# Kernel tuning notes

Measured on AMD Instinct MI355X. Metric: run time of the kernel, lower is better.

Reference implementation:

```python
import jax, jax.numpy as jnp
import numpy as np

V, D, C, H = 32, 128, 2048, 8
B, M = 8, 2048
HD = D // H


def rms_norm(x, scale):
    # Whole-tensor (per-batch) RMS over dims (1,2), as in the source (quirky but faithful).
    Bx, Mx, Dx = x.shape
    fr = jnp.sqrt(jnp.sum(x * x, axis=(1, 2))) * (Mx * Dx) ** -0.5  # (B,)
    raw = x / fr[:, None, None]
    return scale[:Mx, :][None, :, :] * raw


def rope_tables(Mx):
    i = jnp.arange(D // 2, dtype=jnp.float32)
    # NOTE: faithful to source: exponent uses (i-1), not i.
    base = jnp.power(10000.0, -2.0 * (i - 1.0) / D)  # (D/2,)
    pos = jnp.arange(Mx, dtype=jnp.float32)
    ang = pos[:, None] * base[None, :]  # (M, D/2)
    return jnp.cos(ang), jnp.sin(ang)


def apply_rope(t, cos, sin):
    # Equivalent to bmm with the block-diagonal 2x2 rotation matrices:
    # out[2i]   =  t[2i]*cos + t[2i+1]*sin
    # out[2i+1] = -t[2i]*sin + t[2i+1]*cos
    te, to = t[..., 0::2], t[..., 1::2]
    oe = te * cos + to * sin
    oo = -te * sin + to * cos
    return jnp.stack([oe, oo], axis=-1).reshape(t.shape)


def mha(q, k, v, in_w, in_b, out_w, out_b):
    Bx, Mx, _ = q.shape
    qp = q @ in_w[:D].T + in_b[:D]
    kp = k @ in_w[D:2 * D].T + in_b[D:2 * D]
    vp = v @ in_w[2 * D:].T + in_b[2 * D:]
    qh = qp.reshape(Bx, Mx, H, HD).transpose(0, 2, 1, 3)
    kh = kp.reshape(Bx, Mx, H, HD).transpose(0, 2, 1, 3)
    vh = vp.reshape(Bx, Mx, H, HD).transpose(0, 2, 1, 3)
    scores = jnp.einsum('bhqd,bhkd->bhqk', qh, kh) / jnp.sqrt(jnp.float32(HD))
    causal = jnp.tril(jnp.ones((Mx, Mx), dtype=bool))
    scores = jnp.where(causal[None, None], scores, -jnp.inf)
    probs = jax.nn.softmax(scores, axis=-1)  # dropout=0.1 in train mode; eval here
    o = jnp.einsum('bhqk,bhkd->bhqd', probs, vh)
    o = o.transpose(0, 2, 1, 3).reshape(Bx, Mx, D)
    return o @ out_w.T + out_b


def setup_inputs():
    key = jax.random.key(0)
    ks = jax.random.split(key, 12)
    s = 0.02
    return {
        'idx': jax.random.randint(ks[0], (B, M), 0, V),
        'targets': jax.random.randint(ks[1], (B, M), 0, V),
        'emb': jax.random.normal(ks[2], (V, D), jnp.float32) * s,
        'rms_scale': jnp.ones((C, D), jnp.float32),
        'Wq': jax.random.normal(ks[3], (D, D), jnp.float32) * s,
        'Wk': jax.random.normal(ks[4], (D, D), jnp.float32) * s,
        'Wv': jax.random.normal(ks[5], (D, D), jnp.float32) * s,
        'in_proj_w': jax.random.normal(ks[6], (3 * D, D), jnp.float32) * s,
        'in_proj_b': jnp.zeros((3 * D,), jnp.float32),
        'out_proj_w': jax.random.normal(ks[7], (D, D), jnp.float32) * s,
        'out_proj_b': jnp.zeros((D,), jnp.float32),
        'lin_w': jax.random.normal(ks[8], (D, D), jnp.float32) * s,
        'lin_b': jnp.zeros((D,), jnp.float32),
        'out_w': jax.random.normal(ks[9], (V, D), jnp.float32) * s,
        'out_b': jnp.zeros((V,), jnp.float32),
    }


def reference(idx, targets, emb, rms_scale, Wq, Wk, Wv, in_proj_w, in_proj_b,
              out_proj_w, out_proj_b, lin_w, lin_b, out_w, out_b):
    x = emb[idx]                                  # (B, M, D)
    x = rms_norm(x, rms_scale)
    Q = x @ Wq.T
    K = x @ Wk.T
    Vv = x @ Wv.T
    cos, sin = rope_tables(x.shape[1])
    q_out = apply_rope(Q, cos, sin)
    k_out = apply_rope(K, cos, sin)
    v_out = apply_rope(Vv, cos, sin)              # source rotates V too (faithful)
    x = x + mha(q_out, k_out, v_out, in_proj_w, in_proj_b, out_proj_w, out_proj_b)
    x = rms_norm(x, rms_scale)
    x = x + jax.nn.relu(x @ lin_w.T + lin_b)
    logits = x @ out_w.T + out_b                  # (B, M, V)
    logp = jax.nn.log_softmax(logits, axis=-1)
    nll = -jnp.take_along_axis(logp, targets[..., None], axis=-1)[..., 0]
    loss = jnp.mean(nll)
    return logits, loss
```

## Files before the change

kernel.cpp:

```cpp
#include <hip/hip_runtime.h>
#include <hip/hip_bf16.h>
#include <math.h>

#define Vv   32
#define Dd   128
#define Hh   8
#define Bb   8
#define Mm   2048
#define BM   (Bb*Mm)
#define NEL  (BM*Dd)
#define XNS  140
#define QKS  396

typedef _Float16 half4_t __attribute__((ext_vector_type(4)));
typedef _Float16 half8_t __attribute__((ext_vector_type(8)));
typedef __fp16   fp16x2  __attribute__((ext_vector_type(2)));
typedef float    float4_t __attribute__((ext_vector_type(4)));
#define MFMA16 __builtin_amdgcn_mfma_f32_16x16x16f16
#define MFMA32 __builtin_amdgcn_mfma_f32_16x16x32_f16

#if __has_builtin(__builtin_amdgcn_exp2f)
__device__ __forceinline__ float fexp2(float x) { return __builtin_amdgcn_exp2f(x); }
#else
__device__ __forceinline__ float fexp2(float x) { return __expf(x * 0.6931471805599453f); }
#endif

__global__ __launch_bounds__(256) void front_kernel(const float* __restrict__ Wq,
                                                    const float* __restrict__ Wk,
                                                    const float* __restrict__ Wv,
                                                    const float* __restrict__ in_w,
                                                    const float* __restrict__ out_pw,
                                                    const float* __restrict__ lin_w,
                                                    const float* __restrict__ out_w,
                                                    _Float16* __restrict__ Wh,
                                                    float* __restrict__ cosT,
                                                    float* __restrict__ sinT,
                                                    const int* __restrict__ idx,
                                                    const float* __restrict__ emb,
                                                    _Float16* __restrict__ Xh,
                                                    float* __restrict__ partials) {
    __shared__ float wsum[4];
    if (blockIdx.x < 1040) {
        int gid = blockIdx.x * 256 + threadIdx.x;
        if (gid < 135168) {
            const float* src;
            int i;
            if (gid < 131072) {
                int seg = gid >> 14; i = gid & 16383;
                src = seg == 0 ? Wq : seg == 1 ? Wk : seg == 2 ? Wv :
                      seg < 6 ? in_w + (size_t)(seg - 3) * 16384 :
                      seg == 6 ? out_pw : lin_w;
            } else { src = out_w; i = gid - 131072; }
            int tile = i >> 8, within = i & 255;
            int nt = tile >> 3, kk = tile & 7;
            int r = within >> 4, cc = within & 15;
            Wh[gid] = (_Float16)src[(nt * 16 + r) * 128 + kk * 16 + cc];
        } else {
            int rid = gid - 135168;
            int i = rid & 63, m = rid >> 6;
            float ex = -2.0f * ((float)i - 1.0f) / 128.0f;
            float basef = expf(ex * 9.210340371976184f);
            float ang = (float)m * basef;
            cosT[rid] = cosf(ang);
            sinT[rid] = sinf(ang);
        }
    } else {
        int blk = blockIdx.x - 1040;
        int gid = blk * 256 + threadIdx.x;
        int token = gid >> 5, t4 = gid & 31;
        float4 x = *(const float4*)(emb + (size_t)idx[token] * 128 + t4 * 4);
        half4_t o;
        o[0] = (_Float16)x.x; o[1] = (_Float16)x.y; o[2] = (_Float16)x.z; o[3] = (_Float16)x.w;
        *(half4_t*)(Xh + (size_t)gid * 4) = o;
        float v = x.x * x.x + x.y * x.y + x.z * x.z + x.w * x.w;
        #pragma unroll
        for (int off = 32; off; off >>= 1) v += __shfl_xor(v, off);
        int lane = threadIdx.x & 63, wave = threadIdx.x >> 6;
        if (lane == 0) wsum[wave] = v;
        __syncthreads();
        if (threadIdx.x == 0) partials[blk] = wsum[0] + wsum[1] + wsum[2] + wsum[3];
    }
}

__global__ __launch_bounds__(256) void gemm_qkvproj_kernel(const _Float16* __restrict__ xh,
                                                           const float* __restrict__ scale,
                                                           const float* __restrict__ part1,
                                                           const _Float16* __restrict__ Whqkv,
                                                           const _Float16* __restrict__ Whin,
                                                           const float* __restrict__ in_b,
                                                           const float* __restrict__ cosT,
                                                           const float* __restrict__ sinT,
                                                           _Float16* __restrict__ xnh,
                                                           _Float16* __restrict__ Qp,
                                                           _Float16* __restrict__ Kp,
                                                           _Float16* __restrict__ Vp) {
    __shared__ _Float16 xn[32 * XNS];
    __shared__ _Float16 qkv[32 * QKS];
    __shared__ float wsum0[4];
    int tid = threadIdx.x;
    int row0 = blockIdx.x * 32;
    {
        float v = part1[(row0 >> 11) * 256 + tid];
        #pragma unroll
        for (int off = 32; off; off >>= 1) v += __shfl_xor(v, off);
        if ((tid & 63) == 0) wsum0[tid >> 6] = v;
    }
    __syncthreads();
    float iv = 512.0f / sqrtf(wsum0[0] + wsum0[1] + wsum0[2] + wsum0[3]);
    {
        #pragma unroll
        for (int it = 0; it < 2; it++) {
            int idx = tid + it * 256;
            int rw = idx >> 4, c8 = (idx & 15) * 8;
            int m = (row0 + rw) & (Mm - 1);
            half8_t x8 = *(const half8_t*)(xh + (size_t)(row0 + rw) * 128 + c8);
            const float* sp = scale + (size_t)m * 128 + c8;
            float4 s0 = *(const float4*)sp;
            float4 s1 = *(const float4*)(sp + 4);
            half8_t o8;
            o8[0] = (_Float16)((float)x8[0] * iv * s0.x);
            o8[1] = (_Float16)((float)x8[1] * iv * s0.y);
            o8[2] = (_Float16)((float)x8[2] * iv * s0.z);
            o8[3] = (_Float16)((float)x8[3] * iv * s0.w);
            o8[4] = (_Float16)((float)x8[4] * iv * s1.x);
            o8[5] = (_Float16)((float)x8[5] * iv * s1.y);
            o8[6] = (_Float16)((float)x8[6] * iv * s1.z);
            o8[7] = (_Float16)((float)x8[7] * iv * s1.w);
            *(half8_t*)(xn + rw * XNS + c8) = o8;
            *(half8_t*)(xnh + (size_t)(row0 + rw) * 128 + c8) = o8;
        }
    }
    __syncthreads();
    int wave = tid >> 6, lane = tid & 63;
    int r = lane & 15, c = lane >> 4;
    int nb = wave * 96;
    int nb16 = wave * 6;
    int aoff = c * 8;
    int boff = r * 16 + (c & 1) * 8;
    int bsel = c >> 1;
    {
        half8_t af[2][4];
        #pragma unroll
        for (int rt = 0; rt < 2; rt++)
            #pragma unroll
            for (int kk = 0; kk < 4; kk++)
                af[rt][kk] = *(const half8_t*)(xn + (rt * 16 + r) * XNS + kk * 32 + aoff);
        float4_t acc[2][6];
        #pragma unroll
        for (int rt = 0; rt < 2; rt++)
            #pragma unroll
            for (int t = 0; t < 6; t++) acc[rt][t] = (float4_t){0.f, 0.f, 0.f, 0.f};
        #pragma unroll
        for (int kk = 0; kk < 4; kk++) {
            half8_t wf[6];
            #pragma unroll
            for (int t = 0; t < 6; t++)
                wf[t] = *(const half8_t*)(Whqkv + ((nb16 + t) * 8 + kk * 2 + bsel) * 256 + boff);
            #pragma unroll
            for (int t = 0; t < 6; t++) {
                acc[0][t] = MFMA32(af[0][kk], wf[t], acc[0][t], 0, 0, 0);
                acc[1][t] = MFMA32(af[1][kk], wf[t], acc[1][t], 0, 0, 0);
            }
        }
        #pragma unroll
        for (int rt = 0; rt < 2; rt++) {
            #pragma unroll
            for (int t = 0; t < 6; t++) {
                int n = nb + t * 16 + r;
                int ci = (n & 127) >> 1;
                #pragma unroll
                for (int reg = 0; reg < 4; reg++) {
                    int m2 = (row0 + rt * 16 + 4 * c + reg) & (Mm - 1);
                    float v = acc[rt][t][reg];
                    float vp = __shfl_xor(v, 1);
                    float cs = cosT[m2 * 64 + ci], sn = sinT[m2 * 64 + ci];
                    v = (n & 1) ? (-vp * sn + v * cs) : (v * cs + vp * sn);
                    qkv[(rt * 16 + 4 * c + reg) * QKS + n] = (_Float16)v;
                }
            }
        }
    }
    __syncthreads();
    {
        int seg_lo = nb >> 7;
        int seg_hi = (nb + 80) >> 7;
        half8_t aql[2][4], aqh[2][4];
        #pragma unroll
        for (int rt = 0; rt < 2; rt++)
            #pragma unroll
            for (int kk = 0; kk < 4; kk++) {
                aql[rt][kk] = *(const half8_t*)(qkv + (rt * 16 + r) * QKS + seg_lo * 128 + kk * 32 + aoff);
                aqh[rt][kk] = *(const half8_t*)(qkv + (rt * 16 + r) * QKS + seg_hi * 128 + kk * 32 + aoff);
            }
        float4_t acc[2][6];
        #pragma unroll
        for (int rt = 0; rt < 2; rt++)
            #pragma unroll
            for (int t = 0; t < 6; t++) acc[rt][t] = (float4_t){0.f, 0.f, 0.f, 0.f};
        #pragma unroll
        for (int kk = 0; kk < 4; kk++) {
            half8_t wf[6];
            #pragma unroll
            for (int t = 0; t < 6; t++) {
                int colg = nb + t * 16;
                int seg = colg >> 7;
                int ntl = (colg & 127) >> 4;
                wf[t] = *(const half8_t*)(Whin + ((seg * 8 + ntl) * 8 + kk * 2 + bsel) * 256 + boff);
            }
            #pragma unroll
            for (int t = 0; t < 6; t++) {
                int seg = (nb + t * 16) >> 7;
                acc[0][t] = MFMA32(seg == seg_lo ? aql[0][kk] : aqh[0][kk], wf[t], acc[0][t], 0, 0, 0);
                acc[1][t] = MFMA32(seg == seg_lo ? aql[1][kk] : aqh[1][kk], wf[t], acc[1][t], 0, 0, 0);
            }
        }
        int bb = row0 >> 11;
        #pragma unroll
        for (int rt = 0; rt < 2; rt++) {
            int t16 = ((row0 + rt * 16) & 2047) >> 4;
            #pragma unroll
            for (int t = 0; t < 6; t++) {
                int colg = nb + t * 16;
                int seg = colg >> 7;
                int h = (colg & 127) >> 4;
                size_t tb = ((size_t)(bb * 8 + h) * 128 + t16) * 256;
                float bv = in_b[colg + r];
                _Float16* dst = seg == 0 ? Qp : seg == 1 ? Kp : Vp;
                #pragma unroll
                for (int reg = 0; reg < 4; reg++) {
                    float v = acc[rt][t][reg] + bv;
                    int key = 4 * c + reg;
                    if (seg < 2) dst[tb + key * 16 + r] = (_Float16)v;
                    else         dst[tb + r * 16 + key] = (_Float16)v;
                }
            }
        }
    }
}

__global__ __launch_bounds__(256) void gemm_ep1_kernel(const _Float16* __restrict__ Oh,
                                                       const _Float16* __restrict__ W6,
                                                       const float* __restrict__ bias,
                                                       const _Float16* __restrict__ xnh,
                                                       _Float16* __restrict__ xresh,
                                                       float* __restrict__ partials) {
    __shared__ _Float16 At[32 * XNS];
    int tid = threadIdx.x;
    int row0 = blockIdx.x * 32;
    #pragma unroll
    for (int it = 0; it < 2; it++) {
        int idx = tid + it * 256;
        int rw = idx >> 4, c8 = (idx & 15) * 8;
        *(half8_t*)(At + rw * XNS + c8) = *(const half8_t*)(Oh + (size_t)(row0 + rw) * 128 + c8);
    }
    __syncthreads();
    int wave = tid >> 6, lane = tid & 63;
    int r = lane & 15, c = lane >> 4;
    int aoff = c * 8;
    int boff = r * 16 + (c & 1) * 8;
    int bsel = c >> 1;
    int n0 = wave * 32;
    half8_t af[2][4];
    #pragma unroll
    for (int rt = 0; rt < 2; rt++)
        #pragma unroll
        for (int kk = 0; kk < 4; kk++)
            af[rt][kk] = *(const half8_t*)(At + (rt * 16 + r) * XNS + kk * 32 + aoff);
    float4_t acc[2][2];
    #pragma unroll
    for (int rt = 0; rt < 2; rt++) {
        acc[rt][0] = (float4_t){0.f, 0.f, 0.f, 0.f};
        acc[rt][1] = (float4_t){0.f, 0.f, 0.f, 0.f};
    }
    #pragma unroll
    for (int kk = 0; kk < 4; kk++) {
        half8_t wf[2];
        wf[0] = *(const half8_t*)(W6 + ((wave * 2 + 0) * 8 + kk * 2 + bsel) * 256 + boff);
        wf[1] = *(const half8_t*)(W6 + ((wave * 2 + 1) * 8 + kk * 2 + bsel) * 256 + boff);
        #pragma unroll
        for (int t = 0; t < 2; t++) {
            acc[0][t] = MFMA32(af[0][kk], wf[t], acc[0][t], 0, 0, 0);
            acc[1][t] = MFMA32(af[1][kk], wf[t], acc[1][t], 0, 0, 0);
        }
    }
    float lssq = 0.f;
    #pragma unroll
    for (int rt = 0; rt < 2; rt++) {
        #pragma unroll
        for (int t = 0; t < 2; t++) {
            int n = n0 + t * 16 + r;
            float bv = bias[n];
            #pragma unroll
            for (int reg = 0; reg < 4; reg++) {
                int row = row0 + rt * 16 + 4 * c + reg;
                float v = acc[rt][t][reg] + bv + (float)xnh[(size_t)row * 128 + n];
                lssq += v * v;
                xresh[(size_t)row * 128 + n] = (_Float16)v;
            }
        }
    }
    #pragma unroll
    for (int off = 32; off; off >>= 1) lssq += __shfl_xor(lssq, off);
    __shared__ float wsum[4];
    if (lane == 0) wsum[wave] = lssq;
    __syncthreads();
    if (tid == 0) partials[blockIdx.x] = wsum[0] + wsum[1] + wsum[2] + wsum[3];
}

__global__ __launch_bounds__(256) void gemm_ep2_kernel(const _Float16* __restrict__ xresh,
                                                       const float* __restrict__ scale,
                                                       const float* __restrict__ part2,
                                                       const _Float16* __restrict__ W7,
                                                       const float* __restrict__ bias,
                                                       _Float16* __restrict__ ffoh) {
    __shared__ _Float16 At[32 * XNS];
    int tid = threadIdx.x;
    int row0 = blockIdx.x * 32;
    float pv = part2[(row0 >> 11) * 64 + (tid & 63)];
    #pragma unroll
    for (int off = 32; off; off >>= 1) pv += __shfl_xor(pv, off);
    float iv = 512.0f / sqrtf(pv);
    #pragma unroll
    for (int it = 0; it < 2; it++) {
        int idx = tid + it * 256;
        int rw = idx >> 4, c8 = (idx & 15) * 8;
        int m = (row0 + rw) & (Mm - 1);
        half8_t x8 = *(const half8_t*)(xresh + (size_t)(row0 + rw) * 128 + c8);
        const float* sp = scale + (size_t)m * 128 + c8;
        float4 s0 = *(const float4*)sp;
        float4 s1 = *(const float4*)(sp + 4);
        half8_t o8;
        o8[0] = (_Float16)((float)x8[0] * iv * s0.x);
        o8[1] = (_Float16)((float)x8[1] * iv * s0.y);
        o8[2] = (_Float16)((float)x8[2] * iv * s0.z);
        o8[3] = (_Float16)((float)x8[3] * iv * s0.w);
        o8[4] = (_Float16)((float)x8[4] * iv * s1.x);
        o8[5] = (_Float16)((float)x8[5] * iv * s1.y);
        o8[6] = (_Float16)((float)x8[6] * iv * s1.z);
        o8[7] = (_Float16)((float)x8[7] * iv * s1.w);
        *(half8_t*)(At + rw * XNS + c8) = o8;
    }
    __syncthreads();
    int wave = tid >> 6, lane = tid & 63;
    int r = lane & 15, c = lane >> 4;
    int aoff = c * 8;
    int boff = r * 16 + (c & 1) * 8;
    int bsel = c >> 1;
    int n0 = wave * 32;
    half8_t af[2][4];
    #pragma unroll
    for (int rt = 0; rt < 2; rt++)
        #pragma unroll
        for (int kk = 0; kk < 4; kk++)
            af[rt][kk] = *(const half8_t*)(At + (rt * 16 + r) * XNS + kk * 32 + aoff);
    float4_t acc[2][2];
    #pragma unroll
    for (int rt = 0; rt < 2; rt++) {
        acc[rt][0] = (float4_t){0.f, 0.f, 0.f, 0.f};
        acc[rt][1] = (float4_t){0.f, 0.f, 0.f, 0.f};
    }
    #pragma unroll
    for (int kk = 0; kk < 4; kk++) {
        half8_t wf[2];
        wf[0] = *(const half8_t*)(W7 + ((wave * 2 + 0) * 8 + kk * 2 + bsel) * 256 + boff);
        wf[1] = *(const half8_t*)(W7 + ((wave * 2 + 1) * 8 + kk * 2 + bsel) * 256 + boff);
        #pragma unroll
        for (int t = 0; t < 2; t++) {
            acc[0][t] = MFMA32(af[0][kk], wf[t], acc[0][t], 0, 0, 0);
            acc[1][t] = MFMA32(af[1][kk], wf[t], acc[1][t], 0, 0, 0);
        }
    }
    #pragma unroll
    for (int rt = 0; rt < 2; rt++) {
        #pragma unroll
        for (int t = 0; t < 2; t++) {
            int n = n0 + t * 16 + r;
            float bv = bias[n];
            #pragma unroll
            for (int reg = 0; reg < 4; reg++) {
                int row = row0 + rt * 16 + 4 * c + reg;
                float v = fmaxf(acc[rt][t][reg] + bv, 0.f) + (float)xresh[(size_t)row * 128 + n];
                ffoh[(size_t)row * 128 + n] = (_Float16)v;
            }
        }
    }
}

__device__ __forceinline__ half4_t attn_exps(float4_t st, float& ls) {
    float p0 = fexp2(st[0]), p1 = fexp2(st[1]);
    float p2 = fexp2(st[2]), p3 = fexp2(st[3]);
    ls += (p0 + p1) + (p2 + p3);
    fp16x2 lo = __builtin_amdgcn_cvt_pkrtz(p0, p1);
    fp16x2 hi = __builtin_amdgcn_cvt_pkrtz(p2, p3);
    half4_t pf;
    pf[0] = (_Float16)lo[0]; pf[1] = (_Float16)lo[1];
    pf[2] = (_Float16)hi[0]; pf[3] = (_Float16)hi[1];
    return pf;
}
__device__ __forceinline__ half4_t attn_exps_masked(float4_t st, float& ls, int r, int c) {
    float p0 = (4 * c + 0 <= r) ? fexp2(st[0]) : 0.f;
    float p1 = (4 * c + 1 <= r) ? fexp2(st[1]) : 0.f;
    float p2 = (4 * c + 2 <= r) ? fexp2(st[2]) : 0.f;
    float p3 = (4 * c + 3 <= r) ? fexp2(st[3]) : 0.f;
    ls += (p0 + p1) + (p2 + p3);
    fp16x2 lo = __builtin_amdgcn_cvt_pkrtz(p0, p1);
    fp16x2 hi = __builtin_amdgcn_cvt_pkrtz(p2, p3);
    half4_t pf;
    pf[0] = (_Float16)lo[0]; pf[1] = (_Float16)lo[1];
    pf[2] = (_Float16)hi[0]; pf[3] = (_Float16)hi[1];
    return pf;
}

__global__ __launch_bounds__(256) void attn_kernel(const _Float16* __restrict__ Qp,
                                                   const _Float16* __restrict__ Kp,
                                                   const _Float16* __restrict__ Vp,
                                                   _Float16* __restrict__ Oh) {
    __shared__ float mrg[2][10][64];
    int wave = threadIdx.x >> 6, lane = threadIdx.x & 63;
    int pair = blockIdx.x * 2 + (wave >> 1);
    int split = wave & 1;
    int qa = pair & 63, bh = pair >> 6, qb = 127 - qa;
    int r = lane & 15, c = lane >> 4;
    int lofs = r * 16 + 4 * c;
    const _Float16* Kb = Kp + (size_t)bh * 32768 + lofs;
    const _Float16* Vb = Vp + (size_t)bh * 32768 + lofs;
    const _Float16* Qb = Qp + (size_t)bh * 32768 + lofs;
    half4_t qfa = *(const half4_t*)(Qb + qa * 256);
    half4_t qfb = *(const half4_t*)(Qb + qb * 256);
    const _Float16 qscale = (_Float16)0.36067376f;
    qfa *= qscale;
    qfb *= qscale;
    float4_t zero = {0.f, 0.f, 0.f, 0.f};
    float4_t oa = zero, ob = zero;
    float lsa = 0.f, lsb = 0.f;

    for (int kt = split; kt < qa; kt += 2) {
        half4_t k0 = *(const half4_t*)(Kb + (size_t)kt * 256);
        half4_t v0 = *(const half4_t*)(Vb + (size_t)kt * 256);
        float4_t sa = MFMA16(k0, qfa, zero, 0, 0, 0);
        float4_t sb = MFMA16(k0, qfb, zero, 0, 0, 0);
        half4_t pa = attn_exps(sa, lsa);
        half4_t pb = attn_exps(sb, lsb);
        oa = MFMA16(pa, v0, oa, 0, 0, 0);
        ob = MFMA16(pb, v0, ob, 0, 0, 0);
    }
    if ((qa & 1) == split) {
        half4_t k0 = *(const half4_t*)(Kb + (size_t)qa * 256);
        half4_t v0 = *(const half4_t*)(Vb + (size_t)qa * 256);
        float4_t sa = MFMA16(k0, qfa, zero, 0, 0, 0);
        float4_t sb = MFMA16(k0, qfb, zero, 0, 0, 0);
        half4_t pa = attn_exps_masked(sa, lsa, r, c);
        half4_t pb = attn_exps(sb, lsb);
        oa = MFMA16(pa, v0, oa, 0, 0, 0);
        ob = MFMA16(pb, v0, ob, 0, 0, 0);
    }
    {
        int s = qa + 1;
        if ((s & 1) != split) s++;
        for (int kt = s; kt < qb; kt += 2) {
            half4_t k0 = *(const half4_t*)(Kb + (size_t)kt * 256);
            half4_t v0 = *(const half4_t*)(Vb + (size_t)kt * 256);
            float4_t sb = MFMA16(k0, qfb, zero, 0, 0, 0);
            half4_t pb = attn_exps(sb, lsb);
            ob = MFMA16(pb, v0, ob, 0, 0, 0);
        }
    }
    if ((qb & 1) == split) {
        half4_t k0 = *(const half4_t*)(Kb + (size_t)qb * 256);
        half4_t v0 = *(const half4_t*)(Vb + (size_t)qb * 256);
        float4_t sb = MFMA16(k0, qfb, zero, 0, 0, 0);
        half4_t pb = attn_exps_masked(sb, lsb, r, c);
        ob = MFMA16(pb, v0, ob, 0, 0, 0);
    }
    int pib = wave >> 1;
    if (split == 1) {
        #pragma unroll
        for (int i = 0; i < 4; i++) {
            mrg[pib][i][lane] = oa[i];
            mrg[pib][4 + i][lane] = ob[i];
        }
        mrg[pib][8][lane] = lsa;
        mrg[pib][9][lane] = lsb;
    }
    __syncthreads();
    if (split == 0) {
        #pragma unroll
        for (int i = 0; i < 4; i++) {
            oa[i] += mrg[pib][i][lane];
            ob[i] += mrg[pib][4 + i][lane];
        }
        lsa += mrg[pib][8][lane];
        lsb += mrg[pib][9][lane];
        lsa += __shfl_xor(lsa, 16); lsa += __shfl_xor(lsa, 32);
        lsb += __shfl_xor(lsb, 16); lsb += __shfl_xor(lsb, 32);
        int b = bh >> 3, h = bh & 7;
        #pragma unroll
        for (int reg = 0; reg < 4; reg++) {
            float la = __shfl(lsa, 4 * c + reg);
            float lb = __shfl(lsb, 4 * c + reg);
            Oh[(size_t)(b * Mm + qa * 16 + 4 * c + reg) * 128 + h * 16 + r] = (_Float16)(oa[reg] / la);
            Oh[(size_t)(b * Mm + qb * 16 + 4 * c + reg) * 128 + h * 16 + r] = (_Float16)(ob[reg] / lb);
        }
    }
}

__global__ __launch_bounds__(256) void logits_loss_kernel(const _Float16* __restrict__ Xh,
                                                          const _Float16* __restrict__ Wo16,
                                                          const float* __restrict__ bo,
                                                          const int* __restrict__ targets,
                                                          float* __restrict__ logits,
                                                          float* __restrict__ nllPart) {
    __shared__ _Float16 At[64 * XNS];
    __shared__ float wn[4];
    int tid = threadIdx.x;
    int rowb = blockIdx.x * 64;
    #pragma unroll
    for (int it = 0; it < 4; it++) {
        int idx = tid + it * 256;
        int rw = idx >> 4, c8 = (idx & 15) * 8;
        *(half8_t*)(At + rw * XNS + c8) = *(const half8_t*)(Xh + (size_t)(rowb + rw) * 128 + c8);
    }
    __syncthreads();
    int wave = tid >> 6, lane = tid & 63;
    int r = lane & 15, c = lane >> 4;
    int aoff = c * 8;
    int boff = r * 16 + (c & 1) * 8;
    int bsel = c >> 1;
    int row0 = rowb + wave * 16;
    half8_t af[4];
    #pragma unroll
    for (int kk = 0; kk < 4; kk++)
        af[kk] = *(const half8_t*)(At + (wave * 16 + r) * XNS + kk * 32 + aoff);
    float4_t acc[2];
    acc[0] = (float4_t){0.f, 0.f, 0.f, 0.f};
    acc[1] = (float4_t){0.f, 0.f, 0.f, 0.f};
    #pragma unroll
    for (int kk = 0; kk < 4; kk++) {
        #pragma unroll
        for (int t = 0; t < 2; t++) {
            half8_t wf = *(const half8_t*)(Wo16 + (t * 8 + kk * 2 + bsel) * 256 + boff);
            acc[t] = MFMA32(af[kk], wf, acc[t], 0, 0, 0);
        }
    }
    float b0 = bo[r], b1 = bo[r + 16];
    float nll_s = 0.f;
    #pragma unroll
    for (int reg = 0; reg < 4; reg++) {
        int row = row0 + 4 * c + reg;
        float l0 = acc[0][reg] + b0;
        float l1 = acc[1][reg] + b1;
        logits[(size_t)row * 32 + r] = l0;
        logits[(size_t)row * 32 + 16 + r] = l1;
        float mx = fmaxf(l0, l1);
        #pragma unroll
        for (int off = 8; off; off >>= 1) mx = fmaxf(mx, __shfl_xor(mx, off));
        float se = __expf(l0 - mx) + __expf(l1 - mx);
        #pragma unroll
        for (int off = 8; off; off >>= 1) se += __shfl_xor(se, off);
        int tgt = targets[row];
        float sel = (tgt & 16) ? l1 : l0;
        float tval = __shfl(sel, (lane & 48) | (tgt & 15));
        nll_s += logf(se) + mx - tval;
    }
    nll_s += __shfl_xor(nll_s, 16);
    nll_s += __shfl_xor(nll_s, 32);
    if (lane == 0) wn[wave] = nll_s;
    __syncthreads();
    if (tid == 0) nllPart[blockIdx.x] = (wn[0] + wn[1]) + (wn[2] + wn[3]);
}

__global__ __launch_bounds__(256) void loss_reduce_kernel(const float* __restrict__ nllPart,
                                                          float* __restrict__ out) {
    int t = threadIdx.x;
    __shared__ double sh[256];
    sh[t] = (double)nllPart[t];
    __syncthreads();
    for (int off = 128; off; off >>= 1) {
        if (t < off) sh[t] += sh[t + off];
        __syncthreads();
    }
    if (t == 0) out[0] = (float)(sh[0] * (1.0 / (double)BM));
}

extern "C" void kernel_launch(void* const* d_in, const int* in_sizes, int n_in,
                              void* d_out, int out_size, void* d_ws, size_t ws_size,
                              hipStream_t stream) {
    const int*   idx       = (const int*)d_in[0];
    const int*   targets   = (const int*)d_in[1];
    const float* emb       = (const float*)d_in[2];
    const float* rms_scale = (const float*)d_in[3];
    const float* Wq        = (const float*)d_in[4];
    const float* Wk        = (const float*)d_in[5];
    const float* Wv        = (const float*)d_in[6];
    const float* in_w      = (const float*)d_in[7];
    const float* in_b      = (const float*)d_in[8];
    const float* out_pw    = (const float*)d_in[9];
    const float* out_pb    = (const float*)d_in[10];
    const float* lin_w     = (const float*)d_in[11];
    const float* lin_b     = (const float*)d_in[12];
    const float* out_w     = (const float*)d_in[13];
    const float* out_b     = (const float*)d_in[14];
    float* out = (float*)d_out;

    char* base = (char*)d_ws;
    const size_t MB = 1024 * 1024;
    _Float16* xh16  = (_Float16*)base;
    _Float16* xnh   = (_Float16*)(base + 4 * MB);
    _Float16* Oh    = (_Float16*)(base + 8 * MB);
    _Float16* xresh = (_Float16*)(base + 12 * MB);
    _Float16* ffoh  = (_Float16*)(base + 16 * MB);
    _Float16* Qp    = (_Float16*)(base + 20 * MB);
    _Float16* Kp    = (_Float16*)(base + 24 * MB);
    _Float16* Vp    = (_Float16*)(base + 28 * MB);
    float*    cosT  = (float*)(base + 32 * MB);
    float*    sinT  = cosT + Mm * 64;
    float*    part1 = sinT + Mm * 64;
    float*    part2 = part1 + 2048;
    _Float16* Wh    = (_Float16*)(part2 + 512);
    float*    nllBuf = (float*)(Wh + 135168);

    front_kernel<<<1040 + 2048, 256, 0, stream>>>(Wq, Wk, Wv, in_w, out_pw, lin_w, out_w,
                                                  Wh, cosT, sinT, idx, emb, xh16, part1);

    gemm_qkvproj_kernel<<<BM / 32, 256, 0, stream>>>(xh16, rms_scale, part1,
                                                     Wh, Wh + 3 * 16384, in_b,
                                                     cosT, sinT, xnh, Qp, Kp, Vp);

    attn_kernel<<<4096 / 2, 256, 0, stream>>>(Qp, Kp, Vp, Oh);

    gemm_ep1_kernel<<<BM / 32, 256, 0, stream>>>(Oh, Wh + 6 * 16384, out_pb, xnh, xresh, part2);
    gemm_ep2_kernel<<<BM / 32, 256, 0, stream>>>(xresh, rms_scale, part2, Wh + 7 * 16384, lin_b, ffoh);

    logits_loss_kernel<<<BM / 64, 256, 0, stream>>>(ffoh, Wh + 131072, out_b, targets, out, nllBuf);
    loss_reduce_kernel<<<1, 256, 0, stream>>>(nllBuf, out + (size_t)BM * Vv);
}
```

Measured before the change: 160.4 us.

## Widen projection GEMM blocks to 512 threads and fold loss reduction into atomics

The three small projection GEMM kernels now launch 512 threads per block, with each wave computing half as many output columns. They reload A fragments from LDS per k-step instead of caching them in registers, which cuts register pressure and raises occupancy. The separate single-block loss-reduce kernel is removed: each logits block atomically adds its scaled partial NLL into the output, and front_kernel zeroes that slot first. This saves one launch, but the float atomic sum is order-nondeterministic and loses the double-precision accumulation.

New measurement: 154.6 us. 3.6% less time.

```diff
diff --git a/kernel.cpp b/kernel.cpp
--- a/kernel.cpp
+++ b/kernel.cpp
@@ -38,9 +38,11 @@
                                                     const int* __restrict__ idx,
                                                     const float* __restrict__ emb,
                                                     _Float16* __restrict__ Xh,
-                                                    float* __restrict__ partials) {
+                                                    float* __restrict__ partials,
+                                                    float* __restrict__ lossOut) {
     __shared__ float wsum[4];
     if (blockIdx.x < 1040) {
+        if (blockIdx.x == 0 && threadIdx.x == 0) lossOut[0] = 0.f;
         int gid = blockIdx.x * 256 + threadIdx.x;
         if (gid < 135168) {
             const float* src;
@@ -82,90 +84,82 @@
     }
 }
 
-__global__ __launch_bounds__(256) void gemm_qkvproj_kernel(const _Float16* __restrict__ xh,
-                                                           const float* __restrict__ scale,
-                                                           const float* __restrict__ part1,
-                                                           const _Float16* __restrict__ Whqkv,
-                                                           const _Float16* __restrict__ Whin,
-                                                           const float* __restrict__ in_b,
-                                                           const float* __restrict__ cosT,
-                                                           const float* __restrict__ sinT,
-                                                           _Float16* __restrict__ xnh,
-                                                           _Float16* __restrict__ Qp,
-                                                           _Float16* __restrict__ Kp,
-                                                           _Float16* __restrict__ Vp) {
+__global__ __launch_bounds__(512, 4) void gemm_qkvproj_kernel(const _Float16* __restrict__ xh,
+                                                              const float* __restrict__ scale,
+                                                              const float* __restrict__ part1,
+                                                              const _Float16* __restrict__ Whqkv,
+                                                              const _Float16* __restrict__ Whin,
+                                                              const float* __restrict__ in_b,
+                                                              const float* __restrict__ cosT,
+                                                              const float* __restrict__ sinT,
+                                                              _Float16* __restrict__ xnh,
+                                                              _Float16* __restrict__ Qp,
+                                                              _Float16* __restrict__ Kp,
+                                                              _Float16* __restrict__ Vp) {
     __shared__ _Float16 xn[32 * XNS];
     __shared__ _Float16 qkv[32 * QKS];
-    __shared__ float wsum0[4];
+    __shared__ float wsum0[8];
     int tid = threadIdx.x;
     int row0 = blockIdx.x * 32;
     {
-        float v = part1[(row0 >> 11) * 256 + tid];
+        float v = (tid < 256) ? part1[(row0 >> 11) * 256 + tid] : 0.f;
         #pragma unroll
         for (int off = 32; off; off >>= 1) v += __shfl_xor(v, off);
         if ((tid & 63) == 0) wsum0[tid >> 6] = v;
     }
     __syncthreads();
-    float iv = 512.0f / sqrtf(wsum0[0] + wsum0[1] + wsum0[2] + wsum0[3]);
-    {
-        #pragma unroll
-        for (int it = 0; it < 2; it++) {
-            int idx = tid + it * 256;
-            int rw = idx >> 4, c8 = (idx & 15) * 8;
-            int m = (row0 + rw) & (Mm - 1);
-            half8_t x8 = *(const half8_t*)(xh + (size_t)(row0 + rw) * 128 + c8);
-            const float* sp = scale + (size_t)m * 128 + c8;
-            float4 s0 = *(const float4*)sp;
-            float4 s1 = *(const float4*)(sp + 4);
-            half8_t o8;
-            o8[0] = (_Float16)((float)x8[0] * iv * s0.x);
-            o8[1] = (_Float16)((float)x8[1] * iv * s0.y);
-            o8[2] = (_Float16)((float)x8[2] * iv * s0.z);
-            o8[3] = (_Float16)((float)x8[3] * iv * s0.w);
-            o8[4] = (_Float16)((float)x8[4] * iv * s1.x);
-            o8[5] = (_Float16)((float)x8[5] * iv * s1.y);
-            o8[6] = (_Float16)((float)x8[6] * iv * s1.z);
-            o8[7] = (_Float16)((float)x8[7] * iv * s1.w);
-            *(half8_t*)(xn + rw * XNS + c8) = o8;
-            *(half8_t*)(xnh + (size_t)(row0 + rw) * 128 + c8) = o8;
-        }
+    float iv = 512.0f / sqrtf(((wsum0[0] + wsum0[1]) + (wsum0[2] + wsum0[3])) +
+                              ((wsum0[4] + wsum0[5]) + (wsum0[6] + wsum0[7])));
+    {
+        int rw = tid >> 4, c8 = (tid & 15) * 8;
+        int m = (row0 + rw) & (Mm - 1);
+        half8_t x8 = *(const half8_t*)(xh + (size_t)(row0 + rw) * 128 + c8);
+        const float* sp = scale + (size_t)m * 128 + c8;
+        float4 s0 = *(const float4*)sp;
+        float4 s1 = *(const float4*)(sp + 4);
+        half8_t o8;
+        o8[0] = (_Float16)((float)x8[0] * iv * s0.x);
+        o8[1] = (_Float16)((float)x8[1] * iv * s0.y);
+        o8[2] = (_Float16)((float)x8[2] * iv * s0.z);
+        o8[3] = (_Float16)((float)x8[3] * iv * s0.w);
+        o8[4] = (_Float16)((float)x8[4] * iv * s1.x);
+        o8[5] = (_Float16)((float)x8[5] * iv * s1.y);
+        o8[6] = (_Float16)((float)x8[6] * iv * s1.z);
+        o8[7] = (_Float16)((float)x8[7] * iv * s1.w);
+        *(half8_t*)(xn + rw * XNS + c8) = o8;
+        *(half8_t*)(xnh + (size_t)(row0 + rw) * 128 + c8) = o8;
     }
     __syncthreads();
     int wave = tid >> 6, lane = tid & 63;
     int r = lane & 15, c = lane >> 4;
-    int nb = wave * 96;
-    int nb16 = wave * 6;
+    int nb = wave * 48;
     int aoff = c * 8;
     int boff = r * 16 + (c & 1) * 8;
     int bsel = c >> 1;
     {
-        half8_t af[2][4];
+        float4_t acc[2][3];
         #pragma unroll
         for (int rt = 0; rt < 2; rt++)
             #pragma unroll
-            for (int kk = 0; kk < 4; kk++)
-                af[rt][kk] = *(const half8_t*)(xn + (rt * 16 + r) * XNS + kk * 32 + aoff);
-        float4_t acc[2][6];
-        #pragma unroll
-        for (int rt = 0; rt < 2; rt++)
-            #pragma unroll
-            for (int t = 0; t < 6; t++) acc[rt][t] = (float4_t){0.f, 0.f, 0.f, 0.f};
+            for (int t = 0; t < 3; t++) acc[rt][t] = (float4_t){0.f, 0.f, 0.f, 0.f};
         #pragma unroll
         for (int kk = 0; kk < 4; kk++) {
-            half8_t wf[6];
-            #pragma unroll
-            for (int t = 0; t < 6; t++)
-                wf[t] = *(const half8_t*)(Whqkv + ((nb16 + t) * 8 + kk * 2 + bsel) * 256 + boff);
-            #pragma unroll
-            for (int t = 0; t < 6; t++) {
-                acc[0][t] = MFMA32(af[0][kk], wf[t], acc[0][t], 0, 0, 0);
-                acc[1][t] = MFMA32(af[1][kk], wf[t], acc[1][t], 0, 0, 0);
+            half8_t a0 = *(const half8_t*)(xn + r * XNS + kk * 32 + aoff);
+            half8_t a1 = *(const half8_t*)(xn + (16 + r) * XNS + kk * 32 + aoff);
+            half8_t wf[3];
+            #pragma unroll
+            for (int t = 0; t < 3; t++)
+                wf[t] = *(const half8_t*)(Whqkv + ((wave * 3 + t) * 8 + kk * 2 + bsel) * 256 + boff);
+            #pragma unroll
+            for (int t = 0; t < 3; t++) {
+                acc[0][t] = MFMA32(a0, wf[t], acc[0][t], 0, 0, 0);
+                acc[1][t] = MFMA32(a1, wf[t], acc[1][t], 0, 0, 0);
             }
         }
         #pragma unroll
         for (int rt = 0; rt < 2; rt++) {
             #pragma unroll
-            for (int t = 0; t < 6; t++) {
+            for (int t = 0; t < 3; t++) {
                 int n = nb + t * 16 + r;
                 int ci = (n & 127) >> 1;
                 #pragma unroll
@@ -183,35 +177,27 @@
     __syncthreads();
     {
         int seg_lo = nb >> 7;
-        int seg_hi = (nb + 80) >> 7;
-        half8_t aql[2][4], aqh[2][4];
+        int seg_hi = (nb + 32) >> 7;
+        float4_t acc[2][3];
         #pragma unroll
         for (int rt = 0; rt < 2; rt++)
             #pragma unroll
-            for (int kk = 0; kk < 4; kk++) {
-                aql[rt][kk] = *(const half8_t*)(qkv + (rt * 16 + r) * QKS + seg_lo * 128 + kk * 32 + aoff);
-                aqh[rt][kk] = *(const half8_t*)(qkv + (rt * 16 + r) * QKS + seg_hi * 128 + kk * 32 + aoff);
-            }
-        float4_t acc[2][6];
-        #pragma unroll
-        for (int rt = 0; rt < 2; rt++)
-            #pragma unroll
-            for (int t = 0; t < 6; t++) acc[rt][t] = (float4_t){0.f, 0.f, 0.f, 0.f};
+            for (int t = 0; t < 3; t++) acc[rt][t] = (float4_t){0.f, 0.f, 0.f, 0.f};
         #pragma unroll
         for (int kk = 0; kk < 4; kk++) {
-            half8_t wf[6];
-            #pragma unroll
-            for (int t = 0; t < 6; t++) {
+            half8_t al0 = *(const half8_t*)(qkv + r * QKS + seg_lo * 128 + kk * 32 + aoff);
+            half8_t al1 = *(const half8_t*)(qkv + (16 + r) * QKS + seg_lo * 128 + kk * 32 + aoff);
+            half8_t ah0 = *(const half8_t*)(qkv + r * QKS + seg_hi * 128 + kk * 32 + aoff);
+            half8_t ah1 = *(const half8_t*)(qkv + (16 + r) * QKS + seg_hi * 128 + kk * 32 + aoff);
+            #pragma unroll
+            for (int t = 0; t < 3; t++) {
                 int colg = nb + t * 16;
                 int seg = colg >> 7;
                 int ntl = (colg & 127) >> 4;
-                wf[t] = *(const half8_t*)(Whin + ((seg * 8 + ntl) * 8 + kk * 2 + bsel) * 256 + boff);
-            }
-            #pragma unroll
-            for (int t = 0; t < 6; t++) {
-                int seg = (nb + t * 16) >> 7;
-                acc[0][t] = MFMA32(seg == seg_lo ? aql[0][kk] : aqh[0][kk], wf[t], acc[0][t], 0, 0, 0);
-                acc[1][t] = MFMA32(seg == seg_lo ? aql[1][kk] : aqh[1][kk], wf[t], acc[1][t], 0, 0, 0);
+                half8_t wf = *(const half8_t*)(Whin + ((seg * 8 + ntl) * 8 + kk * 2 + bsel) * 256 + boff);
+                bool lo = (seg == seg_lo);
+                acc[0][t] = MFMA32(lo ? al0 : ah0, wf, acc[0][t], 0, 0, 0);
+                acc[1][t] = MFMA32(lo ? al1 : ah1, wf, acc[1][t], 0, 0, 0);
             }
         }
         int bb = row0 >> 11;
@@ -219,7 +205,7 @@
         for (int rt = 0; rt < 2; rt++) {
             int t16 = ((row0 + rt * 16) & 2047) >> 4;
             #pragma unroll
-            for (int t = 0; t < 6; t++) {
+            for (int t = 0; t < 3; t++) {
                 int colg = nb + t * 16;
                 int seg = colg >> 7;
                 int h = (colg & 127) >> 4;
@@ -238,19 +224,17 @@
     }
 }
 
-__global__ __launch_bounds__(256) void gemm_ep1_kernel(const _Float16* __restrict__ Oh,
-                                                       const _Float16* __restrict__ W6,
-                                                       const float* __restrict__ bias,
-                                                       const _Float16* __restrict__ xnh,
-                                                       _Float16* __restrict__ xresh,
-                                                       float* __restrict__ partials) {
+__global__ __launch_bounds__(512, 4) void gemm_ep1_kernel(const _Float16* __restrict__ Oh,
+                                                          const _Float16* __restrict__ W6,
+                                                          const float* __restrict__ bias,
+                                                          const _Float16* __restrict__ xnh,
+                                                          _Float16* __restrict__ xresh,
+                                                          float* __restrict__ partials) {
     __shared__ _Float16 At[32 * XNS];
     int tid = threadIdx.x;
     int row0 = blockIdx.x * 32;
-    #pragma unroll
-    for (int it = 0; it < 2; it++) {
-        int idx = tid + it * 256;
-        int rw = idx >> 4, c8 = (idx & 15) * 8;
+    {
+        int rw = tid >> 4, c8 = (tid & 15) * 8;
         *(half8_t*)(At + rw * XNS + c8) = *(const half8_t*)(Oh + (size_t)(row0 + rw) * 128 + c8);
     }
     __syncthreads();
@@ -259,60 +243,46 @@
     int aoff = c * 8;
     int boff = r * 16 + (c & 1) * 8;
     int bsel = c >> 1;
-    int n0 = wave * 32;
-    half8_t af[2][4];
-    #pragma unroll
-    for (int rt = 0; rt < 2; rt++)
-        #pragma unroll
-        for (int kk = 0; kk < 4; kk++)
-            af[rt][kk] = *(const half8_t*)(At + (rt * 16 + r) * XNS + kk * 32 + aoff);
-    float4_t acc[2][2];
+    int n0 = wave * 16;
+    float4_t acc[2];
+    acc[0] = (float4_t){0.f, 0.f, 0.f, 0.f};
+    acc[1] = (float4_t){0.f, 0.f, 0.f, 0.f};
+    #pragma unroll
+    for (int kk = 0; kk < 4; kk++) {
+        half8_t a0 = *(const half8_t*)(At + r * XNS + kk * 32 + aoff);
+        half8_t a1 = *(const half8_t*)(At + (16 + r) * XNS + kk * 32 + aoff);
+        half8_t wf = *(const half8_t*)(W6 + (wave * 8 + kk * 2 + bsel) * 256 + boff);
+        acc[0] = MFMA32(a0, wf, acc[0], 0, 0, 0);
+        acc[1] = MFMA32(a1, wf, acc[1], 0, 0, 0);
+    }
+    float lssq = 0.f;
+    int n = n0 + r;
+    float bv = bias[n];
     #pragma unroll
     for (int rt = 0; rt < 2; rt++) {
-        acc[rt][0] = (float4_t){0.f, 0.f, 0.f, 0.f};
-        acc[rt][1] = (float4_t){0.f, 0.f, 0.f, 0.f};
-    }
-    #pragma unroll
-    for (int kk = 0; kk < 4; kk++) {
-        half8_t wf[2];
-        wf[0] = *(const half8_t*)(W6 + ((wave * 2 + 0) * 8 + kk * 2 + bsel) * 256 + boff);
-        wf[1] = *(const half8_t*)(W6 + ((wave * 2 + 1) * 8 + kk * 2 + bsel) * 256 + boff);
-        #pragma unroll
-        for (int t = 0; t < 2; t++) {
-            acc[0][t] = MFMA32(af[0][kk], wf[t], acc[0][t], 0, 0, 0);
-            acc[1][t] = MFMA32(af[1][kk], wf[t], acc[1][t], 0, 0, 0);
-        }
-    }
-    float lssq = 0.f;
-    #pragma unroll
-    for (int rt = 0; rt < 2; rt++) {
-        #pragma unroll
-        for (int t = 0; t < 2; t++) {
-            int n = n0 + t * 16 + r;
-            float bv = bias[n];
-            #pragma unroll
-            for (int reg = 0; reg < 4; reg++) {
-                int row = row0 + rt * 16 + 4 * c + reg;
-                float v = acc[rt][t][reg] + bv + (float)xnh[(size_t)row * 128 + n];
-                lssq += v * v;
-                xresh[(size_t)row * 128 + n] = (_Float16)v;
-            }
+        #pragma unroll
+        for (int reg = 0; reg < 4; reg++) {
+            int row = row0 + rt * 16 + 4 * c + reg;
+            float v = acc[rt][reg] + bv + (float)xnh[(size_t)row * 128 + n];
+            lssq += v * v;
+            xresh[(size_t)row * 128 + n] = (_Float16)v;
         }
     }
     #pragma unroll
     for (int off = 32; off; off >>= 1) lssq += __shfl_xor(lssq, off);
-    __shared__ float wsum[4];
+    __shared__ float wsum[8];
     if (lane == 0) wsum[wave] = lssq;
     __syncthreads();
-    if (tid == 0) partials[blockIdx.x] = wsum[0] + wsum[1] + wsum[2] + wsum[3];
-}
-
-__global__ __launch_bounds__(256) void gemm_ep2_kernel(const _Float16* __restrict__ xresh,
-                                                       const float* __restrict__ scale,
-                                                       const float* __restrict__ part2,
-                                                       const _Float16* __restrict__ W7,
-                                                       const float* __restrict__ bias,
-                                                       _Float16* __restrict__ ffoh) {
+    if (tid == 0) partials[blockIdx.x] = ((wsum[0] + wsum[1]) + (wsum[2] + wsum[3])) +
+                                        ((wsum[4] + wsum[5]) + (wsum[6] + wsum[7]));
+}
+
+__global__ __launch_bounds__(512, 4) void gemm_ep2_kernel(const _Float16* __restrict__ xresh,
+                                                          const float* __restrict__ scale,
+                                                          const float* __restrict__ part2,
+                                                          const _Float16* __restrict__ W7,
+                                                          const float* __restrict__ bias,
+                                                          _Float16* __restrict__ ffoh) {
     __shared__ _Float16 At[32 * XNS];
     int tid = threadIdx.x;
     int row0 = blockIdx.x * 32;
@@ -320,10 +290,8 @@
     #pragma unroll
     for (int off = 32; off; off >>= 1) pv += __shfl_xor(pv, off);
     float iv = 512.0f / sqrtf(pv);
-    #pragma unroll
-    for (int it = 0; it < 2; it++) {
-        int idx = tid + it * 256;
-        int rw = idx >> 4, c8 = (idx & 15) * 8;
+    {
+        int rw = tid >> 4, c8 = (tid & 15) * 8;
         int m = (row0 + rw) & (Mm - 1);
         half8_t x8 = *(const half8_t*)(xresh + (size_t)(row0 + rw) * 128 + c8);
         const float* sp = scale + (size_t)m * 128 + c8;
@@ -346,42 +314,27 @@
     int aoff = c * 8;
     int boff = r * 16 + (c & 1) * 8;
     int bsel = c >> 1;
-    int n0 = wave * 32;
-    half8_t af[2][4];
-    #pragma unroll
-    for (int rt = 0; rt < 2; rt++)
-        #pragma unroll
-        for (int kk = 0; kk < 4; kk++)
-            af[rt][kk] = *(const half8_t*)(At + (rt * 16 + r) * XNS + kk * 32 + aoff);
-    float4_t acc[2][2];
+    int n0 = wave * 16;
+    float4_t acc[2];
+    acc[0] = (float4_t){0.f, 0.f, 0.f, 0.f};
+    acc[1] = (float4_t){0.f, 0.f, 0.f, 0.f};
+    #pragma unroll
+    for (int kk = 0; kk < 4; kk++) {
+        half8_t a0 = *(const half8_t*)(At + r * XNS + kk * 32 + aoff);
+        half8_t a1 = *(const half8_t*)(At + (16 + r) * XNS + kk * 32 + aoff);
+        half8_t wf = *(const half8_t*)(W7 + (wave * 8 + kk * 2 + bsel) * 256 + boff);
+        acc[0] = MFMA32(a0, wf, acc[0], 0, 0, 0);
+        acc[1] = MFMA32(a1, wf, acc[1], 0, 0, 0);
+    }
+    int n = n0 + r;
+    float bv = bias[n];
     #pragma unroll
     for (int rt = 0; rt < 2; rt++) {
-        acc[rt][0] = (float4_t){0.f, 0.f, 0.f, 0.f};
-        acc[rt][1] = (float4_t){0.f, 0.f, 0.f, 0.f};
-    }
-    #pragma unroll
-    for (int kk = 0; kk < 4; kk++) {
-        half8_t wf[2];
-        wf[0] = *(const half8_t*)(W7 + ((wave * 2 + 0) * 8 + kk * 2 + bsel) * 256 + boff);
-        wf[1] = *(const half8_t*)(W7 + ((wave * 2 + 1) * 8 + kk * 2 + bsel) * 256 + boff);
-        #pragma unroll
-        for (int t = 0; t < 2; t++) {
-            acc[0][t] = MFMA32(af[0][kk], wf[t], acc[0][t], 0, 0, 0);
-            acc[1][t] = MFMA32(af[1][kk], wf[t], acc[1][t], 0, 0, 0);
-        }
-    }
-    #pragma unroll
-    for (int rt = 0; rt < 2; rt++) {
-        #pragma unroll
-        for (int t = 0; t < 2; t++) {
-            int n = n0 + t * 16 + r;
-            float bv = bias[n];
-            #pragma unroll
-            for (int reg = 0; reg < 4; reg++) {
-                int row = row0 + rt * 16 + 4 * c + reg;
-                float v = fmaxf(acc[rt][t][reg] + bv, 0.f) + (float)xresh[(size_t)row * 128 + n];
-                ffoh[(size_t)row * 128 + n] = (_Float16)v;
-            }
+        #pragma unroll
+        for (int reg = 0; reg < 4; reg++) {
+            int row = row0 + rt * 16 + 4 * c + reg;
+            float v = fmaxf(acc[rt][reg] + bv, 0.f) + (float)xresh[(size_t)row * 128 + n];
+            ffoh[(size_t)row * 128 + n] = (_Float16)v;
         }
     }
 }
@@ -509,7 +462,7 @@
                                                           const float* __restrict__ bo,
                                                           const int* __restrict__ targets,
                                                           float* __restrict__ logits,
-                                                          float* __restrict__ nllPart) {
+                                                          float* __restrict__ lossOut) {
     __shared__ _Float16 At[64 * XNS];
     __shared__ float wn[4];
     int tid = threadIdx.x;
@@ -566,20 +519,7 @@
     nll_s += __shfl_xor(nll_s, 32);
     if (lane == 0) wn[wave] = nll_s;
     __syncthreads();
-    if (tid == 0) nllPart[blockIdx.x] = (wn[0] + wn[1]) + (wn[2] + wn[3]);
-}
-
-__global__ __launch_bounds__(256) void loss_reduce_kernel(const float* __restrict__ nllPart,
-                                                          float* __restrict__ out) {
-    int t = threadIdx.x;
-    __shared__ double sh[256];
-    sh[t] = (double)nllPart[t];
-    __syncthreads();
-    for (int off = 128; off; off >>= 1) {
-        if (t < off) sh[t] += sh[t + off];
-        __syncthreads();
-    }
-    if (t == 0) out[0] = (float)(sh[0] * (1.0 / (double)BM));
+    if (tid == 0) atomicAdd(lossOut, ((wn[0] + wn[1]) + (wn[2] + wn[3])) * (1.0f / (float)BM));
 }
 
 extern "C" void kernel_launch(void* const* d_in, const int* in_sizes, int n_in,
@@ -601,6 +541,7 @@
     const float* out_w     = (const float*)d_in[13];
     const float* out_b     = (const float*)d_in[14];
     float* out = (float*)d_out;
+    float* lossOut = out + (size_t)BM * Vv;
 
     char* base = (char*)d_ws;
     const size_t MB = 1024 * 1024;
@@ -617,20 +558,18 @@
     float*    part1 = sinT + Mm * 64;
     float*    part2 = part1 + 2048;
     _Float16* Wh    = (_Float16*)(part2 + 512);
-    float*    nllBuf = (float*)(Wh + 135168);
 
     front_kernel<<<1040 + 2048, 256, 0, stream>>>(Wq, Wk, Wv, in_w, out_pw, lin_w, out_w,
-                                                  Wh, cosT, sinT, idx, emb, xh16, part1);
-
-    gemm_qkvproj_kernel<<<BM / 32, 256, 0, stream>>>(xh16, rms_scale, part1,
+                                                  Wh, cosT, sinT, idx, emb, xh16, part1, lossOut);
+
+    gemm_qkvproj_kernel<<<BM / 32, 512, 0, stream>>>(xh16, rms_scale, part1,
                                                      Wh, Wh + 3 * 16384, in_b,
                                                      cosT, sinT, xnh, Qp, Kp, Vp);
 
     attn_kernel<<<4096 / 2, 256, 0, stream>>>(Qp, Kp, Vp, Oh);
 
-    gemm_ep1_kernel<<<BM / 32, 256, 0, stream>>>(Oh, Wh + 6 * 16384, out_pb, xnh, xresh, part2);
-    gemm_ep2_kernel<<<BM / 32, 256, 0, stream>>>(xresh, rms_scale, part2, Wh + 7 * 16384, lin_b, ffoh);
-
-    logits_loss_kernel<<<BM / 64, 256, 0, stream>>>(ffoh, Wh + 131072, out_b, targets, out, nllBuf);
-    loss_reduce_kernel<<<1, 256, 0, stream>>>(nllBuf, out + (size_t)BM * Vv);
-}
+    gemm_ep1_kernel<<<BM / 32, 512, 0, stream>>>(Oh, Wh + 6 * 16384, out_pb, xnh, xresh, part2);
+    gemm_ep2_kernel<<<BM / 32, 512, 0, stream>>>(xresh, rms_scale, part2, Wh + 7 * 16384, lin_b, ffoh);
+
+    logits_loss_kernel<<<BM / 64, 256, 0, stream>>>(ffoh, Wh + 131072, out_b, targets, out, lossOut);
+}
```
